# Optimization experiments

Measured on AMD Instinct MI355X. Metric: run time of the kernel, lower is better.

The kernel has to match this reference:

```python
import jax, jax.numpy as jnp
import numpy as np

NEG_INF = -1e15  # matches masked_fill value -1000000000000000.0
ALPHA = 0.2      # leakyReLU negative slope


def setup_inputs() -> dict:
    key = jax.random.key(0)
    k1, k2, k3, k4 = jax.random.split(key, 4)
    N, F_IN, F_OUT = 8192, 256, 64
    x = jax.random.normal(k1, (N, F_IN), dtype=jnp.float32)
    mask = jax.random.randint(k2, (N, N), 0, 2, dtype=jnp.int32)
    trans = jax.random.normal(k3, (F_IN, F_OUT), dtype=jnp.float32) * 0.1
    attn = jax.random.normal(k4, (2 * F_OUT, 1), dtype=jnp.float32) * 0.1
    return {"x": x, "mask": mask, "trans": trans, "attn": attn}


def reference(x, mask, trans, attn):
    d = trans.shape[1]
    h = x @ trans                                  # [N, d]
    e1 = h @ attn[:d, :]                           # [N, 1]
    e2 = h @ attn[d:, :]                           # [N, 1]
    scores = jax.nn.leaky_relu(e1 + e2.T, negative_slope=ALPHA)  # [N, N]
    masked = jnp.where(mask == 0, NEG_INF, scores)
    attention = jax.nn.softmax(masked, axis=1)
    return attention @ h                           # [N, d]
```

## Files before the change

kernel.cpp:

```cpp
#include <hip/hip_runtime.h>
#include <hip/hip_bf16.h>
#include <math.h>

#define N 8192
#define FIN 256
#define D 64
#define ALPHA 0.2f
#define SROW 1040
#define WBUF (16 * SROW)

typedef __attribute__((ext_vector_type(8))) short bf16x8;
typedef __attribute__((ext_vector_type(4))) float f32x4;

__global__ __launch_bounds__(256) void k_h_e(
    const float* __restrict__ x, const float* __restrict__ trans,
    const float* __restrict__ attn,
    __hip_bfloat16* __restrict__ hF, float* __restrict__ e1, float* __restrict__ e2)
{
    __shared__ float xs[8 * FIN];
    __shared__ __hip_bfloat16 hl[8 * D];
    const int t = threadIdx.x;
    const int r0 = blockIdx.x * 8;

    #pragma unroll
    for (int v = 0; v < 2; ++v) {
        int idx = t + 256 * v;
        ((float4*)xs)[idx] = ((const float4*)(x + (size_t)r0 * FIN))[idx];
    }
    __syncthreads();

    const int lane = t & 63, w = t >> 6;
    const float* xa = xs + (2 * w) * FIN;
    const float* xb = xs + (2 * w + 1) * FIN;
    float acca = 0.f, accb = 0.f;
    #pragma unroll 8
    for (int k = 0; k < FIN; ++k) {
        const float tv = trans[k * D + lane];
        acca = fmaf(xa[k], tv, acca);
        accb = fmaf(xb[k], tv, accb);
    }
    const int ra = r0 + 2 * w, rb = ra + 1;

    const float a1 = attn[lane], a2 = attn[D + lane];
    float p1a = acca * a1, p2a = acca * a2;
    float p1b = accb * a1, p2b = accb * a2;
    #pragma unroll
    for (int mm = 1; mm <= 32; mm <<= 1) {
        p1a += __shfl_xor(p1a, mm);
        p2a += __shfl_xor(p2a, mm);
        p1b += __shfl_xor(p1b, mm);
        p2b += __shfl_xor(p2b, mm);
    }
    if (lane == 0) { e1[ra] = p1a; e2[ra] = p2a; e1[rb] = p1b; e2[rb] = p2b; }

    hl[(2 * w) * D + lane]     = __float2bfloat16(acca);
    hl[(2 * w + 1) * D + lane] = __float2bfloat16(accb);
    __syncthreads();
    if (t < D) {
        const int q = t >> 4, m = t & 15;
        const int cb = r0 >> 5, jgrp = (r0 >> 3) & 3;
        union { bf16x8 v; __hip_bfloat16 h[8]; } o;
        #pragma unroll
        for (int r = 0; r < 8; ++r) o.h[r] = hl[r * D + q * 16 + m];
        *(bf16x8*)(hF + (((size_t)cb * 4 + q) * 64 + jgrp * 16 + m) * 8) = o.v;
    }
}

__global__ __launch_bounds__(256) void k_attn(
    const int* __restrict__ mask, const __hip_bfloat16* __restrict__ hF,
    const float* __restrict__ e1, const float* __restrict__ e2,
    float* __restrict__ acc_part, float* __restrict__ l_part, int cs)
{
    __shared__ __align__(16) char smem[4 * WBUF];
    const int t = threadIdx.x;
    const int lane = t & 63, wave = t >> 6;
    const int i0 = (blockIdx.y * 4 + wave) * 16;
    const int sp = blockIdx.x;
    const int c0 = sp * cs;
    const int m = lane & 15, quad = lane >> 4;
    const int row = i0 + m;
    const float er = e1[row];

    char* sw = smem + wave * WBUF;
    const char* swm = sw + m * SROW;
    const __hip_bfloat16* hfp = hF + (((size_t)(c0 >> 5)) * 4 * 64 + lane) * 8;

    f32x4 acc0 = {0.f, 0.f, 0.f, 0.f};
    f32x4 acc1 = {0.f, 0.f, 0.f, 0.f};
    f32x4 acc2 = {0.f, 0.f, 0.f, 0.f};
    f32x4 acc3 = {0.f, 0.f, 0.f, 0.f};
    float lsum = 0.f;

    const int nss = cs >> 8;

    for (int ss = 0; ss < nss; ++ss) {
        const int cb0 = c0 + ss * 256;
        #pragma unroll
        for (int r = 0; r < 16; ++r) {
            const int* g = mask + (size_t)(i0 + r) * N + cb0 + lane * 4;
            char* l = sw + r * SROW + lane * 16;
            __builtin_amdgcn_global_load_lds(
                (const __attribute__((address_space(1))) void*)g,
                (__attribute__((address_space(3))) void*)l, 16, 0, 2 );
        }
        __builtin_amdgcn_s_waitcnt(0x0F70);

        const int itg0 = ss * 8;
        bf16x8 pb0, pb1, pb2, pb3; float4 pea, peb;
        {
            const size_t ito = (size_t)itg0 * 2048;
            pb0 = *(const bf16x8*)(hfp + ito);
            pb1 = *(const bf16x8*)(hfp + ito + 512);
            pb2 = *(const bf16x8*)(hfp + ito + 1024);
            pb3 = *(const bf16x8*)(hfp + ito + 1536);
            const int jb = cb0 + quad * 8;
            pea = *(const float4*)(e2 + jb);
            peb = *(const float4*)(e2 + jb + 4);
        }
        #pragma unroll
        for (int p = 0; p < 8; ++p) {
            const bf16x8 b0 = pb0, b1 = pb1, b2 = pb2, b3 = pb3;
            const float4 ea = pea, eb = peb;
            if (p < 7) {
                const size_t ito = (size_t)(itg0 + p + 1) * 2048;
                pb0 = *(const bf16x8*)(hfp + ito);
                pb1 = *(const bf16x8*)(hfp + ito + 512);
                pb2 = *(const bf16x8*)(hfp + ito + 1024);
                pb3 = *(const bf16x8*)(hfp + ito + 1536);
                const int jb = cb0 + (p + 1) * 32 + quad * 8;
                pea = *(const float4*)(e2 + jb);
                peb = *(const float4*)(e2 + jb + 4);
            }
            const int4 m0 = *(const int4*)(swm + p * 128 + quad * 32);
            const int4 m1 = *(const int4*)(swm + p * 128 + quad * 32 + 16);

            float s0 = er + ea.x; s0 = s0 > 0.f ? s0 : ALPHA * s0;
            float s1 = er + ea.y; s1 = s1 > 0.f ? s1 : ALPHA * s1;
            float s2 = er + ea.z; s2 = s2 > 0.f ? s2 : ALPHA * s2;
            float s3 = er + ea.w; s3 = s3 > 0.f ? s3 : ALPHA * s3;
            float s4 = er + eb.x; s4 = s4 > 0.f ? s4 : ALPHA * s4;
            float s5 = er + eb.y; s5 = s5 > 0.f ? s5 : ALPHA * s5;
            float s6 = er + eb.z; s6 = s6 > 0.f ? s6 : ALPHA * s6;
            float s7 = er + eb.w; s7 = s7 > 0.f ? s7 : ALPHA * s7;
            const float p0 = m0.x ? __expf(s0) : 0.f;
            const float p1 = m0.y ? __expf(s1) : 0.f;
            const float p2 = m0.z ? __expf(s2) : 0.f;
            const float p3 = m0.w ? __expf(s3) : 0.f;
            const float p4 = m1.x ? __expf(s4) : 0.f;
            const float p5 = m1.y ? __expf(s5) : 0.f;
            const float p6 = m1.z ? __expf(s6) : 0.f;
            const float p7 = m1.w ? __expf(s7) : 0.f;

            union { bf16x8 v; __hip_bfloat162 h2[4]; } af;
            af.h2[0] = __float22bfloat162_rn(make_float2(p0, p1));
            af.h2[1] = __float22bfloat162_rn(make_float2(p2, p3));
            af.h2[2] = __float22bfloat162_rn(make_float2(p4, p5));
            af.h2[3] = __float22bfloat162_rn(make_float2(p6, p7));

            lsum += ((p0 + p1) + (p2 + p3)) + ((p4 + p5) + (p6 + p7));

            acc0 = __builtin_amdgcn_mfma_f32_16x16x32_bf16(af.v, b0, acc0, 0, 0, 0);
            acc1 = __builtin_amdgcn_mfma_f32_16x16x32_bf16(af.v, b1, acc1, 0, 0, 0);
            acc2 = __builtin_amdgcn_mfma_f32_16x16x32_bf16(af.v, b2, acc2, 0, 0, 0);
            acc3 = __builtin_amdgcn_mfma_f32_16x16x32_bf16(af.v, b3, acc3, 0, 0, 0);
        }
    }

    lsum += __shfl_xor(lsum, 16);
    lsum += __shfl_xor(lsum, 32);
    if (quad == 0) l_part[(size_t)sp * N + row] = lsum;

    #pragma unroll
    for (int reg = 0; reg < 4; ++reg) {
        const size_t rbase = ((size_t)sp * N + i0 + quad * 4 + reg) * D;
        acc_part[rbase + m     ] = acc0[reg];
        acc_part[rbase + m + 16] = acc1[reg];
        acc_part[rbase + m + 32] = acc2[reg];
        acc_part[rbase + m + 48] = acc3[reg];
    }
}

__global__ __launch_bounds__(256) void k_reduce(
    const float* __restrict__ acc_part, const float* __restrict__ l_part,
    float* __restrict__ out, int nsplit)
{
    const int idx = blockIdx.x * 256 + threadIdx.x;
    const int row = idx >> 6;
    float sum = 0.f, l = 0.f;
    for (int s = 0; s < nsplit; ++s) {
        sum += acc_part[(size_t)s * N * D + idx];
        l   += l_part[(size_t)s * N + row];
    }
    out[idx] = sum / l;
}

extern "C" void kernel_launch(void* const* d_in, const int* in_sizes, int n_in,
                              void* d_out, int out_size, void* d_ws, size_t ws_size,
                              hipStream_t stream) {
    const float* x     = (const float*)d_in[0];
    const int*   mask  = (const int*)d_in[1];
    const float* trans = (const float*)d_in[2];
    const float* attn  = (const float*)d_in[3];
    float* out = (float*)d_out;

    char* ws = (char*)d_ws;
    __hip_bfloat16* hF = (__hip_bfloat16*)ws;
    char* p = ws + (size_t)D * N * sizeof(__hip_bfloat16);
    float* e1 = (float*)p;            p += (size_t)N * sizeof(float);
    float* e2 = (float*)p;            p += (size_t)N * sizeof(float);

    const size_t used = (size_t)(p - ws);
    int nsplit = 4;
    while (nsplit > 1) {
        size_t need = used + (size_t)nsplit * N * sizeof(float)
                    + (size_t)nsplit * N * D * sizeof(float);
        if (need <= ws_size) break;
        nsplit >>= 1;
    }
    float* l_part = (float*)p;
    float* acc_part = l_part + (size_t)nsplit * N;

    k_h_e<<<N / 8, 256, 0, stream>>>(x, trans, attn, hF, e1, e2);
    dim3 g2(nsplit, N / 64);
    k_attn<<<g2, 256, 0, stream>>>(mask, hF, e1, e2, acc_part, l_part, N / nsplit);
    k_reduce<<<(N * D) / 256, 256, 0, stream>>>(acc_part, l_part, out, nsplit);
}
```

Before: 384.0 us.

## Fuse split-K reduction into attention kernel via in-block LDS combine

Reassigns the column splits to the four waves of one block, each covering the same 16 rows, and combines their partial accumulators and row sums in shared memory before writing the normalized output. This removes the separate reduction kernel launch and the global round trip of partial accumulators. Per-block work layout changes, and there is an extra block-wide synchronization and an LDS reduction at the end.

```diff
diff --git a/kernel.cpp b/kernel.cpp
--- a/kernel.cpp
+++ b/kernel.cpp
@@ -8,6 +8,7 @@
 #define ALPHA 0.2f
 #define SROW 1040
 #define WBUF (16 * SROW)
+#define CS 2048
 
 typedef __attribute__((ext_vector_type(8))) short bf16x8;
 typedef __attribute__((ext_vector_type(4))) float f32x4;
@@ -69,14 +70,14 @@
 __global__ __launch_bounds__(256) void k_attn(
     const int* __restrict__ mask, const __hip_bfloat16* __restrict__ hF,
     const float* __restrict__ e1, const float* __restrict__ e2,
-    float* __restrict__ acc_part, float* __restrict__ l_part, int cs)
+    float* __restrict__ out)
 {
     __shared__ __align__(16) char smem[4 * WBUF];
+    __shared__ float lw[4][16];
     const int t = threadIdx.x;
     const int lane = t & 63, wave = t >> 6;
-    const int i0 = (blockIdx.y * 4 + wave) * 16;
-    const int sp = blockIdx.x;
-    const int c0 = sp * cs;
+    const int i0 = blockIdx.x * 16;
+    const int c0 = wave * CS;
     const int m = lane & 15, quad = lane >> 4;
     const int row = i0 + m;
     const float er = e1[row];
@@ -91,7 +92,7 @@
     f32x4 acc3 = {0.f, 0.f, 0.f, 0.f};
     float lsum = 0.f;
 
-    const int nss = cs >> 8;
+    const int nss = CS >> 8;
 
     for (int ss = 0; ss < nss; ++ss) {
         const int cb0 = c0 + ss * 256;
@@ -168,30 +169,28 @@
 
     lsum += __shfl_xor(lsum, 16);
     lsum += __shfl_xor(lsum, 32);
-    if (quad == 0) l_part[(size_t)sp * N + row] = lsum;
-
+    if (quad == 0) lw[wave][m] = lsum;
+
+    __syncthreads();
+    float* cw = (float*)smem;
     #pragma unroll
     for (int reg = 0; reg < 4; ++reg) {
-        const size_t rbase = ((size_t)sp * N + i0 + quad * 4 + reg) * D;
-        acc_part[rbase + m     ] = acc0[reg];
-        acc_part[rbase + m + 16] = acc1[reg];
-        acc_part[rbase + m + 32] = acc2[reg];
-        acc_part[rbase + m + 48] = acc3[reg];
-    }
-}
-
-__global__ __launch_bounds__(256) void k_reduce(
-    const float* __restrict__ acc_part, const float* __restrict__ l_part,
-    float* __restrict__ out, int nsplit)
-{
-    const int idx = blockIdx.x * 256 + threadIdx.x;
-    const int row = idx >> 6;
-    float sum = 0.f, l = 0.f;
-    for (int s = 0; s < nsplit; ++s) {
-        sum += acc_part[(size_t)s * N * D + idx];
-        l   += l_part[(size_t)s * N + row];
-    }
-    out[idx] = sum / l;
+        float* rbase = cw + (wave * 16 + quad * 4 + reg) * 64;
+        rbase[m     ] = acc0[reg];
+        rbase[m + 16] = acc1[reg];
+        rbase[m + 32] = acc2[reg];
+        rbase[m + 48] = acc3[reg];
+    }
+    __syncthreads();
+    #pragma unroll
+    for (int rr = 0; rr < 4; ++rr) {
+        const int idx = rr * 256 + t;
+        const int r = idx >> 6, c = idx & 63;
+        float s = ((cw[(0 * 16 + r) * 64 + c] + cw[(1 * 16 + r) * 64 + c])
+                +   cw[(2 * 16 + r) * 64 + c]) + cw[(3 * 16 + r) * 64 + c];
+        float l = ((lw[0][r] + lw[1][r]) + lw[2][r]) + lw[3][r];
+        out[(size_t)(i0 + r) * D + c] = s / l;
+    }
 }
 
 extern "C" void kernel_launch(void* const* d_in, const int* in_sizes, int n_in,
@@ -209,19 +208,6 @@
     float* e1 = (float*)p;            p += (size_t)N * sizeof(float);
     float* e2 = (float*)p;            p += (size_t)N * sizeof(float);
 
-    const size_t used = (size_t)(p - ws);
-    int nsplit = 4;
-    while (nsplit > 1) {
-        size_t need = used + (size_t)nsplit * N * sizeof(float)
-                    + (size_t)nsplit * N * D * sizeof(float);
-        if (need <= ws_size) break;
-        nsplit >>= 1;
-    }
-    float* l_part = (float*)p;
-    float* acc_part = l_part + (size_t)nsplit * N;
-
     k_h_e<<<N / 8, 256, 0, stream>>>(x, trans, attn, hF, e1, e2);
-    dim3 g2(nsplit, N / 64);
-    k_attn<<<g2, 256, 0, stream>>>(mask, hF, e1, e2, acc_part, l_part, N / nsplit);
-    k_reduce<<<(N * D) / 256, 256, 0, stream>>>(acc_part, l_part, out, nsplit);
+    k_attn<<<N / 16, 256, 0, stream>>>(mask, hF, e1, e2, out);
 }
```

Result: no change. 382.8 us (-0.3%).
